# Performance work log

Measured on AMD Instinct MI355X. Metric: run time of the kernel, lower is better.

Reference implementation:

```python
import jax, jax.numpy as jnp
import numpy as np

S_DIM = 8      # state_dim
O_DIM = 4      # obs_dim
HID = (S_DIM * S_DIM + O_DIM * O_DIM) * 10   # 800
BATCH = 128
SEQ = 32
NS = 16        # num_samples
P_DROP = 0.2
DROP_KEY = jax.random.key(42)

def f_dyn(x):
    # synthetic nonlinear dynamics (stand-in for system_model.f, vmapped over batch)
    return 0.9 * x + 0.1 * jnp.sin(x)

def h_obs(x):
    # synthetic nonlinear observation (stand-in for system_model.h)
    return jnp.tanh(x[..., :O_DIM])

def l2_normalize(x, eps=1e-12):
    # matches torch F.normalize(p=2, dim=1): x / max(||x||, eps)
    n = jnp.linalg.norm(x, axis=-1, keepdims=True)
    return x / jnp.maximum(n, eps)

def setup_inputs() -> dict:
    key = jax.random.key(0)
    ks = jax.random.split(key, 8)
    g = 0.02
    return {
        "y_seq": jax.random.normal(ks[0], (BATCH, SEQ, O_DIM), dtype=jnp.float32),
        "W1": jax.random.normal(ks[1], (HID, S_DIM + O_DIM), dtype=jnp.float32) * g,
        "b1": jnp.zeros((HID,), jnp.float32),
        "W_ih": jax.random.normal(ks[2], (3 * HID, HID), dtype=jnp.float32) * g,
        "W_hh": jax.random.normal(ks[3], (3 * HID, HID), dtype=jnp.float32) * g,
        "b_ih": jnp.zeros((3 * HID,), jnp.float32),
        "b_hh": jnp.zeros((3 * HID,), jnp.float32),
        "W_out": jax.random.normal(ks[4], (S_DIM * O_DIM, HID), dtype=jnp.float32) * g,
        "b_out": jnp.zeros((S_DIM * O_DIM,), jnp.float32),
        "num_samples": NS,
    }

def _forward(y_seq, W1, b1, W_ih, W_hh, b_ih, b_hh, W_out, b_out, num_samples):
    B = y_seq.shape[0]
    keep = 1.0 - P_DROP

    def gru_cell(x, h):
        # torch nn.GRU single-step math; x,h: [..., HID]
        gi = x @ W_ih.T + b_ih
        gh = h @ W_hh.T + b_hh
        gi_r, gi_z, gi_n = jnp.split(gi, 3, axis=-1)
        gh_r, gh_z, gh_n = jnp.split(gh, 3, axis=-1)
        r = jax.nn.sigmoid(gi_r + gh_r)
        z = jax.nn.sigmoid(gi_z + gh_z)
        n = jnp.tanh(gi_n + r * gh_n)
        return (1.0 - z) * n + z * h

    def step(carry, inp):
        x_prev, dx_prev, h_ens = carry            # [B,S], [B,S], [NS,B,HID]
        y_t, t = inp
        x_pred = f_dyn(x_prev)                    # [B,S] (same for every sample j)
        y_hat = h_obs(x_pred)                     # [B,O]
        innov = y_t - y_hat                       # [B,O]
        nn_in = jnp.concatenate([l2_normalize(dx_prev), l2_normalize(innov)], axis=-1)
        a = jax.nn.relu(nn_in @ W1.T + b1)        # [B,HID]
        k1, k2 = jax.random.split(jax.random.fold_in(DROP_KEY, t))
        m1 = jax.random.bernoulli(k1, keep, (num_samples, B, HID)).astype(a.dtype)
        a_ens = a[None] * m1 / keep               # MC-dropout per ensemble member
        h_new = gru_cell(a_ens, h_ens)            # [NS,B,HID] (vectorized over samples)
        K_vec = h_new @ W_out.T + b_out           # [NS,B,S*O]
        m2 = jax.random.bernoulli(k2, keep, K_vec.shape).astype(a.dtype)
        K = (K_vec * m2 / keep).reshape(num_samples, B, S_DIM, O_DIM)
        ens = x_pred[None] + jnp.einsum('jbso,bo->jbs', K, innov)  # [NS,B,S]
        x_filt = ens.mean(axis=0)                 # [B,S]
        diff = ens - x_filt[None]                 # [NS,B,S]
        P_filt = jnp.einsum('jbs,jbt->bst', diff, diff) / num_samples
        dx = x_filt - x_pred                      # delta_x_prev = x_filt - f(x_prev)
        return (x_filt, dx, h_new), (x_filt, P_filt)

    x0 = jnp.zeros((B, S_DIM), y_seq.dtype)
    dx0 = jnp.zeros((B, S_DIM), y_seq.dtype)
    h0 = jnp.zeros((num_samples, B, HID), y_seq.dtype)
    ts = jnp.arange(y_seq.shape[1])
    _, (xs, Ps) = jax.lax.scan(step, (x0, dx0, h0), (jnp.swapaxes(y_seq, 0, 1), ts))
    # xs: [T,B,S] -> [B,T,S]; Ps: [T,B,S,S] -> [B,T,S,S]
    return jnp.swapaxes(xs, 0, 1), jnp.swapaxes(Ps, 0, 1)

def reference(y_seq, W1, b1, W_ih, W_hh, b_ih, b_hh, W_out, b_out, num_samples):
    return _forward(y_seq, W1, b1, W_ih, W_hh, b_ih, b_hh, W_out, b_out, num_samples)
```

## Files before the change

kernel.cpp:

```cpp
#include <hip/hip_runtime.h>
#include <stdint.h>

#define NSAMP 16
#define BATCH 128
#define SEQLEN 32
#define SDIM 8
#define ODIM 4
#define HID 800
#define MROWS (NSAMP * BATCH)
#define KEEPP 0.8f

#define WPK_NBLK 77824
#define WPK_G 12928
#define WPK_C 808
#define GRU_LDS_BYTES 155648

typedef __attribute__((ext_vector_type(8))) short short8v;
typedef __attribute__((ext_vector_type(4))) float float4v;

__host__ __device__ __forceinline__ void tf2x32(uint32_t k0, uint32_t k1,
                                                uint32_t x0, uint32_t x1,
                                                uint32_t& o0, uint32_t& o1) {
  uint32_t ks2 = k0 ^ k1 ^ 0x1BD11BDAu;
  x0 += k0; x1 += k1;
#define TFR(r) { x0 += x1; x1 = (x1 << (r)) | (x1 >> (32 - (r))); x1 ^= x0; }
  TFR(13) TFR(15) TFR(26) TFR(6)
  x0 += k1; x1 += ks2 + 1u;
  TFR(17) TFR(29) TFR(16) TFR(24)
  x0 += ks2; x1 += k0 + 2u;
  TFR(13) TFR(15) TFR(26) TFR(6)
  x0 += k0; x1 += k1 + 3u;
  TFR(17) TFR(29) TFR(16) TFR(24)
  x0 += k1; x1 += ks2 + 4u;
  TFR(13) TFR(15) TFR(26) TFR(6)
  x0 += ks2; x1 += k0 + 5u;
#undef TFR
  o0 = x0; o1 = x1;
}

__device__ __forceinline__ float bits_to_unit(uint32_t bits) {
  return __uint_as_float((bits >> 9) | 0x3F800000u) - 1.0f;
}

__device__ __forceinline__ float tf_uniform_part(uint32_t k0, uint32_t k1, uint32_t idx) {
  uint32_t b1, b2;
  tf2x32(k0, k1, 0u, idx, b1, b2);
  return bits_to_unit(b1 ^ b2);
}

__device__ __forceinline__ ushort f2bf(float f) {
  uint32_t u = __float_as_uint(f);
  uint32_t r = (u + 0x7FFFu + ((u >> 16) & 1u)) >> 16;
  return (ushort)r;
}

__device__ __forceinline__ float bf2f(ushort u) {
  return __uint_as_float((uint32_t)u << 16);
}

__global__ void pack_w_kernel(const float* __restrict__ W_ih, const float* __restrict__ W_hh,
                              ushort* __restrict__ Wpk) {
  const int blk = blockIdx.x;
  const int nblk = blk / 6, g = blk % 6;
  const float* W = (g < 3) ? W_ih : W_hh;
  const int grow = (g % 3) * HID;
  ushort* dst = Wpk + (size_t)nblk * WPK_NBLK + (size_t)g * WPK_G;
  for (int idx = threadIdx.x; idx < 16 * WPK_C; idx += 256) {
    int c = idx / WPK_C, k = idx - c * WPK_C;
    float v = (k < HID) ? W[(size_t)(grow + nblk * 16 + c) * HID + k] : 0.0f;
    dst[c * WPK_C + k] = f2bf(v);
  }
}

__global__ void transpose_wout_kernel(const float* __restrict__ W_out, float* __restrict__ WoutT) {
  int i = blockIdx.x * 256 + threadIdx.x;
  if (i < 32 * HID) {
    int o = i / HID, k = i - o * HID;
    WoutT[k * 32 + o] = W_out[i];
  }
}

__global__ void a_ens_kernel(const float* __restrict__ a, ushort* __restrict__ aeb,
                             uint32_t k0, uint32_t k1) {
  int base = (blockIdx.x * blockDim.x + threadIdx.x) * 4;
  if (base >= MROWS * HID) return;
  int row = base / HID;
  int b = row % BATCH;
  int col = base - row * HID;
  float4 av = *reinterpret_cast<const float4*>(a + b * HID + col);
  ushort4 ov;
#pragma unroll
  for (int q = 0; q < 4; ++q) {
    float u = tf_uniform_part(k0, k1, (uint32_t)(base + q));
    float f = (&av.x)[q] * ((u < KEEPP) ? 1.25f : 0.0f);
    (&ov.x)[q] = f2bf(f);
  }
  *reinterpret_cast<ushort4*>(aeb + base) = ov;
}

__global__ __launch_bounds__(512, 2) void gru_mfma_kernel(
    const ushort* __restrict__ aeb, const ushort* __restrict__ hb,
    const ushort* __restrict__ Wpk,
    const float* __restrict__ h_old,
    const float* __restrict__ b_ih, const float* __restrict__ b_hh,
    float* __restrict__ h_new, ushort* __restrict__ h_new_b) {
  extern __shared__ __align__(16) char lds[];

  const int tid = threadIdx.x;
  const int w = tid >> 6;
  const int lane = tid & 63;
  const int l15 = lane & 15;
  const int kg = lane >> 4;

  const int bid = blockIdx.x;
  const int nhalf = bid >> 3;
  const int r3 = bid & 7;
  const int mblk = r3 >> 1;
  const int nblk = nhalf * 2 + (r3 & 1);
  const int m0 = mblk * 512;
  const int n0 = nblk * 16;

  {
    const ushort* wsrc = Wpk + (size_t)nblk * WPK_NBLK + (size_t)lane * 8;
    for (int s = w * 19; s < w * 19 + 19; ++s) {
      __builtin_amdgcn_global_load_lds(
          (const __attribute__((address_space(1))) void*)(wsrc + (size_t)s * 512),
          (__attribute__((address_space(3))) void*)(lds + s * 1024), 16, 0, 0);
    }
  }

  float4v acc[6][4];
#pragma unroll
  for (int g = 0; g < 6; ++g)
#pragma unroll
    for (int mf = 0; mf < 4; ++mf)
      acc[g][mf] = (float4v)(0.0f);

  const ushort* ap[2][4];
#pragma unroll
  for (int mf = 0; mf < 4; ++mf) {
    const int row = m0 + w * 64 + mf * 16 + l15;
    ap[0][mf] = aeb + (size_t)row * HID + kg * 8;
    ap[1][mf] = hb + (size_t)row * HID + kg * 8;
  }
  short8v ar0[2][4], ar1[2][4];

#define LOADA(SET) do {                                                          \
    _Pragma("unroll")                                                            \
    for (int s2 = 0; s2 < 2; ++s2)                                               \
      _Pragma("unroll")                                                          \
      for (int mf = 0; mf < 4; ++mf) {                                           \
        SET[s2][mf] = *reinterpret_cast<const short8v*>(ap[s2][mf]);             \
        ap[s2][mf] += 32;                                                        \
      }                                                                          \
  } while (0)

#define COMP(T, SET) do {                                                        \
    short8v bfr[6];                                                              \
    _Pragma("unroll")                                                            \
    for (int g = 0; g < 6; ++g)                                                  \
      bfr[g] = *reinterpret_cast<const short8v*>(                                \
          lds + g * 25856 + l15 * 1616 + (T) * 64 + kg * 16);                    \
    __builtin_amdgcn_s_setprio(1);                                               \
    _Pragma("unroll")                                                            \
    for (int g = 0; g < 6; ++g) {                                                \
      const int src = (g < 3) ? 0 : 1;                                           \
      _Pragma("unroll")                                                          \
      for (int mf = 0; mf < 4; ++mf)                                             \
        acc[g][mf] = __builtin_amdgcn_mfma_f32_16x16x32_bf16(                    \
            SET[src][mf], bfr[g], acc[g][mf], 0, 0, 0);                          \
    }                                                                            \
    __builtin_amdgcn_s_setprio(0);                                               \
  } while (0)

  LOADA(ar0);
  asm volatile("s_waitcnt vmcnt(0)" ::: "memory");
  __syncthreads();

#pragma unroll 1
  for (int t = 0; t < 24; t += 2) {
    LOADA(ar1);
    COMP(t, ar0);
    LOADA(ar0);
    COMP(t + 1, ar1);
  }
  COMP(24, ar0);

  const int rowq = (lane >> 4) * 4;
  const int col = n0 + l15;
  const float bir = b_ih[col], biz = b_ih[col + HID], bin = b_ih[col + 2 * HID];
  const float bhr = b_hh[col], bhz = b_hh[col + HID], bhn = b_hh[col + 2 * HID];
#pragma unroll
  for (int mf = 0; mf < 4; ++mf) {
#pragma unroll
    for (int reg = 0; reg < 4; ++reg) {
      const int m = m0 + w * 64 + mf * 16 + rowq + reg;
      float gir = acc[0][mf][reg] + bir;
      float giz = acc[1][mf][reg] + biz;
      float gin = acc[2][mf][reg] + bin;
      float ghr = acc[3][mf][reg] + bhr;
      float ghz = acc[4][mf][reg] + bhz;
      float ghn = acc[5][mf][reg] + bhn;
      float r = 1.0f / (1.0f + expf(-(gir + ghr)));
      float z = 1.0f / (1.0f + expf(-(giz + ghz)));
      float nval = tanhf(gin + r * ghn);
      float hv = h_old[(size_t)m * HID + col];
      float res = (1.0f - z) * nval + z * hv;
      h_new[(size_t)m * HID + col] = res;
      h_new_b[(size_t)m * HID + col] = f2bf(res);
    }
  }
#undef LOADA
#undef COMP
}

__global__ void kvec_ens_kernel(const ushort* __restrict__ hnb,
                                const float* __restrict__ WoutT,
                                const float* __restrict__ b_out,
                                const float* __restrict__ x_pred,
                                const float* __restrict__ innov,
                                float* __restrict__ ens,
                                uint32_t k0, uint32_t k1) {
  const int jb = blockIdx.x;
  const int b = jb & (BATCH - 1);
  const int tid = threadIdx.x;
  const int o = tid & 31;
  const int kk = tid >> 5;

  const ushort* hrow = hnb + (size_t)jb * HID + kk * 100;
  const float* wc = WoutT + kk * 100 * 32 + o;
  float partial = 0.0f;
  for (int k = 0; k < 100; ++k)
    partial = fmaf(bf2f(hrow[k]), wc[k * 32], partial);

  __shared__ float red[8][32];
  __shared__ float Kv[32];
  red[kk][o] = partial;
  __syncthreads();
  if (tid < 32) {
    float s = 0.0f;
#pragma unroll
    for (int q = 0; q < 8; ++q) s += red[q][tid];
    s += b_out[tid];
    float u = tf_uniform_part(k0, k1, (uint32_t)(jb * 32 + tid));
    Kv[tid] = (u < KEEPP) ? s * 1.25f : 0.0f;
  }
  __syncthreads();
  if (tid < SDIM) {
    float s = x_pred[b * SDIM + tid];
#pragma unroll
    for (int oo = 0; oo < ODIM; ++oo)
      s = fmaf(Kv[tid * ODIM + oo], innov[b * ODIM + oo], s);
    ens[jb * SDIM + tid] = s;
  }
}

__global__ void reduce_prep_kernel(const float* __restrict__ ens,
                                   float* __restrict__ x_pred,
                                   float* __restrict__ innov,
                                   const float* __restrict__ y_seq,
                                   const float* __restrict__ W1,
                                   const float* __restrict__ b1,
                                   float* __restrict__ a,
                                   float* __restrict__ out_xs, float* __restrict__ out_Ps,
                                   int t) {
  const int b = blockIdx.x;
  const int tid = threadIdx.x;
  __shared__ float e[NSAMP][SDIM];
  __shared__ float xf[SDIM];
  __shared__ float dxs[SDIM];
  __shared__ float xpn[SDIM];
  __shared__ float inv[ODIM];
  __shared__ float nin[SDIM + ODIM];

  if (t >= 0) {
    if (tid < NSAMP * SDIM) {
      int j = tid >> 3, s = tid & 7;
      e[j][s] = ens[(j * BATCH + b) * SDIM + s];
    }
    __syncthreads();
    if (tid < SDIM) {
      float s = 0.0f;
#pragma unroll
      for (int j = 0; j < NSAMP; ++j) s += e[j][tid];
      s *= (1.0f / NSAMP);
      xf[tid] = s;
      out_xs[(b * SEQLEN + t) * SDIM + tid] = s;
      dxs[tid] = s - x_pred[b * SDIM + tid];
    }
    __syncthreads();
    if (tid < SDIM * SDIM) {
      int s = tid >> 3, u = tid & 7;
      float accv = 0.0f;
#pragma unroll
      for (int j = 0; j < NSAMP; ++j)
        accv += (e[j][s] - xf[s]) * (e[j][u] - xf[u]);
      out_Ps[((b * SEQLEN + t) * SDIM + s) * SDIM + u] = accv * (1.0f / NSAMP);
    }
  } else {
    if (tid < SDIM) { xf[tid] = 0.0f; dxs[tid] = 0.0f; }
  }
  if (t == SEQLEN - 1) return;
  __syncthreads();
  if (tid < SDIM) {
    float x = xf[tid];
    float xp = 0.9f * x + 0.1f * sinf(x);
    xpn[tid] = xp;
    x_pred[b * SDIM + tid] = xp;
  }
  __syncthreads();
  if (tid < ODIM) {
    float yh = tanhf(xpn[tid]);
    float iv = y_seq[(b * SEQLEN + (t + 1)) * ODIM + tid] - yh;
    inv[tid] = iv;
    innov[b * ODIM + tid] = iv;
  }
  __syncthreads();
  if (tid == 0) {
    float nd = 0.0f;
    for (int s = 0; s < SDIM; ++s) nd += dxs[s] * dxs[s];
    nd = fmaxf(sqrtf(nd), 1e-12f);
    for (int s = 0; s < SDIM; ++s) nin[s] = dxs[s] / nd;
    float ni = 0.0f;
    for (int o2 = 0; o2 < ODIM; ++o2) ni += inv[o2] * inv[o2];
    ni = fmaxf(sqrtf(ni), 1e-12f);
    for (int o2 = 0; o2 < ODIM; ++o2) nin[SDIM + o2] = inv[o2] / ni;
  }
  __syncthreads();
  for (int i = tid; i < HID; i += blockDim.x) {
    float s = b1[i];
#pragma unroll
    for (int c = 0; c < 12; ++c) s = fmaf(nin[c], W1[i * 12 + c], s);
    a[b * HID + i] = fmaxf(s, 0.0f);
  }
}

extern "C" void kernel_launch(void* const* d_in, const int* in_sizes, int n_in,
                              void* d_out, int out_size, void* d_ws, size_t ws_size,
                              hipStream_t stream) {
  (void)in_sizes; (void)n_in; (void)out_size; (void)ws_size;
  const float* y_seq = (const float*)d_in[0];
  const float* W1 = (const float*)d_in[1];
  const float* b1 = (const float*)d_in[2];
  const float* W_ih = (const float*)d_in[3];
  const float* W_hh = (const float*)d_in[4];
  const float* b_ih = (const float*)d_in[5];
  const float* b_hh = (const float*)d_in[6];
  const float* W_out = (const float*)d_in[7];
  const float* b_out = (const float*)d_in[8];

  char* ws = (char*)d_ws;
  size_t off = 0;
  float* h_a = (float*)(ws + off);    off += (size_t)MROWS * HID * 4;
  float* h_b = (float*)(ws + off);    off += (size_t)MROWS * HID * 4;
  ushort* hb_a = (ushort*)(ws + off); off += (size_t)MROWS * HID * 2;
  ushort* hb_b = (ushort*)(ws + off); off += (size_t)MROWS * HID * 2;
  ushort* aeb = (ushort*)(ws + off);  off += (size_t)MROWS * HID * 2;
  ushort* Wpk = (ushort*)(ws + off);  off += (size_t)50 * WPK_NBLK * 2;
  float* a_buf = (float*)(ws + off);  off += (size_t)BATCH * HID * 4;
  float* WoutT = (float*)(ws + off);  off += (size_t)HID * 32 * 4;
  float* x_pred = (float*)(ws + off); off += (size_t)BATCH * SDIM * 4;
  float* innov = (float*)(ws + off);  off += (size_t)BATCH * ODIM * 4;
  float* ens = (float*)(ws + off);    off += (size_t)NSAMP * BATCH * SDIM * 4;

  float* out_xs = (float*)d_out;
  float* out_Ps = out_xs + (size_t)BATCH * SEQLEN * SDIM;

  (void)hipFuncSetAttribute(reinterpret_cast<const void*>(&gru_mfma_kernel),
                            hipFuncAttributeMaxDynamicSharedMemorySize, GRU_LDS_BYTES);

  hipMemsetAsync(h_a, 0, (size_t)MROWS * HID * 4, stream);
  hipMemsetAsync(hb_a, 0, (size_t)MROWS * HID * 2, stream);
  pack_w_kernel<<<300, 256, 0, stream>>>(W_ih, W_hh, Wpk);
  transpose_wout_kernel<<<100, 256, 0, stream>>>(W_out, WoutT);
  reduce_prep_kernel<<<BATCH, 256, 0, stream>>>(ens, x_pred, innov, y_seq, W1, b1,
                                                a_buf, out_xs, out_Ps, -1);

  float* hc = h_a;  float* hn = h_b;
  ushort* hcb = hb_a; ushort* hnb = hb_b;
  for (int t = 0; t < SEQLEN; ++t) {
    uint32_t kt0, kt1, k1a, k1b, k2a, k2b;
    tf2x32(0u, 42u, 0u, (uint32_t)t, kt0, kt1);
    tf2x32(kt0, kt1, 0u, 0u, k1a, k1b);
    tf2x32(kt0, kt1, 0u, 1u, k2a, k2b);

    a_ens_kernel<<<1600, 256, 0, stream>>>(a_buf, aeb, k1a, k1b);
    gru_mfma_kernel<<<200, 512, GRU_LDS_BYTES, stream>>>(aeb, hcb, Wpk, hc,
                                                         b_ih, b_hh, hn, hnb);
    kvec_ens_kernel<<<MROWS, 256, 0, stream>>>(hnb, WoutT, b_out, x_pred, innov, ens, k2a, k2b);
    reduce_prep_kernel<<<BATCH, 256, 0, stream>>>(ens, x_pred, innov, y_seq, W1, b1,
                                                  a_buf, out_xs, out_Ps, t);
    float* tmp = hc; hc = hn; hn = tmp;
    ushort* tmpb = hcb; hcb = hnb; hnb = tmpb;
  }
}
```

Baseline: 2.043 ms.

## Store GRU A-operands in MFMA fragment order and deepen load pipeline

```diff
diff --git a/kernel.cpp b/kernel.cpp
--- a/kernel.cpp
+++ b/kernel.cpp
@@ -54,10 +54,6 @@
   return (ushort)r;
 }
 
-__device__ __forceinline__ float bf2f(ushort u) {
-  return __uint_as_float((uint32_t)u << 16);
-}
-
 __global__ void pack_w_kernel(const float* __restrict__ W_ih, const float* __restrict__ W_hh,
                               ushort* __restrict__ Wpk) {
   const int blk = blockIdx.x;
@@ -80,30 +76,39 @@
   }
 }
 
-__global__ void a_ens_kernel(const float* __restrict__ a, ushort* __restrict__ aeb,
+__global__ void a_ens_kernel(const float* __restrict__ a_buf, ushort* __restrict__ AF,
                              uint32_t k0, uint32_t k1) {
-  int base = (blockIdx.x * blockDim.x + threadIdx.x) * 4;
-  if (base >= MROWS * HID) return;
-  int row = base / HID;
-  int b = row % BATCH;
-  int col = base - row * HID;
-  float4 av = *reinterpret_cast<const float4*>(a + b * HID + col);
-  ushort4 ov;
+  const int gw = blockIdx.x * 4 + (threadIdx.x >> 6);
+  const int lane = threadIdx.x & 63;
+  const int mt = gw / 25, kt = gw - mt * 25;
+  const int row = mt * 16 + (lane & 15);
+  const int b = row & (BATCH - 1);
+  const int k = kt * 32 + (lane >> 4) * 8;
+  const float* src = a_buf + (size_t)b * HID + k;
+  float4 v0 = *reinterpret_cast<const float4*>(src);
+  float4 v1 = *reinterpret_cast<const float4*>(src + 4);
+  const uint32_t base = (uint32_t)(row * HID + k);
+  ushort o[8];
 #pragma unroll
   for (int q = 0; q < 4; ++q) {
-    float u = tf_uniform_part(k0, k1, (uint32_t)(base + q));
-    float f = (&av.x)[q] * ((u < KEEPP) ? 1.25f : 0.0f);
-    (&ov.x)[q] = f2bf(f);
-  }
-  *reinterpret_cast<ushort4*>(aeb + base) = ov;
+    float u = tf_uniform_part(k0, k1, base + q);
+    o[q] = f2bf((&v0.x)[q] * ((u < KEEPP) ? 1.25f : 0.0f));
+  }
+#pragma unroll
+  for (int q = 0; q < 4; ++q) {
+    float u = tf_uniform_part(k0, k1, base + 4 + q);
+    o[4 + q] = f2bf((&v1.x)[q] * ((u < KEEPP) ? 1.25f : 0.0f));
+  }
+  *reinterpret_cast<short8v*>(AF + ((size_t)gw * 64 + lane) * 8) =
+      *reinterpret_cast<const short8v*>(o);
 }
 
 __global__ __launch_bounds__(512, 2) void gru_mfma_kernel(
-    const ushort* __restrict__ aeb, const ushort* __restrict__ hb,
+    const ushort* __restrict__ AF, const ushort* __restrict__ HF,
     const ushort* __restrict__ Wpk,
     const float* __restrict__ h_old,
     const float* __restrict__ b_ih, const float* __restrict__ b_hh,
-    float* __restrict__ h_new, ushort* __restrict__ h_new_b) {
+    float* __restrict__ h_new, ushort* __restrict__ hf_out) {
   extern __shared__ __align__(16) char lds[];
 
   const int tid = threadIdx.x;
@@ -119,6 +124,7 @@
   const int nblk = nhalf * 2 + (r3 & 1);
   const int m0 = mblk * 512;
   const int n0 = nblk * 16;
+  const int mtb = mblk * 32;
 
   {
     const ushort* wsrc = Wpk + (size_t)nblk * WPK_NBLK + (size_t)lane * 8;
@@ -139,19 +145,19 @@
   const ushort* ap[2][4];
 #pragma unroll
   for (int mf = 0; mf < 4; ++mf) {
-    const int row = m0 + w * 64 + mf * 16 + l15;
-    ap[0][mf] = aeb + (size_t)row * HID + kg * 8;
-    ap[1][mf] = hb + (size_t)row * HID + kg * 8;
-  }
-  short8v ar0[2][4], ar1[2][4];
+    const size_t mt = (size_t)(mtb + w * 4 + mf);
+    ap[0][mf] = AF + mt * 12800 + (size_t)lane * 8;
+    ap[1][mf] = HF + mt * 12800 + (size_t)lane * 8;
+  }
+  short8v s0[2][4], s1[2][4], s2[2][4];
 
 #define LOADA(SET) do {                                                          \
     _Pragma("unroll")                                                            \
-    for (int s2 = 0; s2 < 2; ++s2)                                               \
+    for (int sx = 0; sx < 2; ++sx)                                               \
       _Pragma("unroll")                                                          \
       for (int mf = 0; mf < 4; ++mf) {                                           \
-        SET[s2][mf] = *reinterpret_cast<const short8v*>(ap[s2][mf]);             \
-        ap[s2][mf] += 32;                                                        \
+        SET[sx][mf] = *reinterpret_cast<const short8v*>(ap[sx][mf]);             \
+        ap[sx][mf] += 512;                                                       \
       }                                                                          \
   } while (0)
 
@@ -173,25 +179,44 @@
     __builtin_amdgcn_s_setprio(0);                                               \
   } while (0)
 
-  LOADA(ar0);
+  LOADA(s0);
+  LOADA(s1);
+  asm volatile("s_waitcnt vmcnt(16)" ::: "memory");
+  __syncthreads();
+
+#pragma unroll 1
+  for (int t = 0; t < 21; t += 3) {
+    LOADA(s2);
+    asm volatile("s_waitcnt vmcnt(16)" ::: "memory");
+    COMP(t, s0);
+    LOADA(s0);
+    asm volatile("s_waitcnt vmcnt(16)" ::: "memory");
+    COMP(t + 1, s1);
+    LOADA(s1);
+    asm volatile("s_waitcnt vmcnt(16)" ::: "memory");
+    COMP(t + 2, s2);
+  }
+  LOADA(s2);
+  asm volatile("s_waitcnt vmcnt(16)" ::: "memory");
+  COMP(21, s0);
+  LOADA(s0);
+  asm volatile("s_waitcnt vmcnt(16)" ::: "memory");
+  COMP(22, s1);
+  asm volatile("s_waitcnt vmcnt(8)" ::: "memory");
+  COMP(23, s2);
   asm volatile("s_waitcnt vmcnt(0)" ::: "memory");
-  __syncthreads();
-
-#pragma unroll 1
-  for (int t = 0; t < 24; t += 2) {
-    LOADA(ar1);
-    COMP(t, ar0);
-    LOADA(ar0);
-    COMP(t + 1, ar1);
-  }
-  COMP(24, ar0);
+  COMP(24, s0);
 
   const int rowq = (lane >> 4) * 4;
   const int col = n0 + l15;
   const float bir = b_ih[col], biz = b_ih[col + HID], bin = b_ih[col + 2 * HID];
   const float bhr = b_hh[col], bhz = b_hh[col + HID], bhn = b_hh[col + 2 * HID];
+  const int khalf = (l15 >> 3) & 1;
+  const int kq = l15 & 7;
 #pragma unroll
   for (int mf = 0; mf < 4; ++mf) {
+    const size_t mt = (size_t)(mtb + w * 4 + mf);
+    ushort* hfw = hf_out + mt * 12800 + (size_t)nblk * 256 + khalf * 128 + kq;
 #pragma unroll
     for (int reg = 0; reg < 4; ++reg) {
       const int m = m0 + w * 64 + mf * 16 + rowq + reg;
@@ -207,14 +232,14 @@
       float hv = h_old[(size_t)m * HID + col];
       float res = (1.0f - z) * nval + z * hv;
       h_new[(size_t)m * HID + col] = res;
-      h_new_b[(size_t)m * HID + col] = f2bf(res);
+      hfw[(rowq + reg) * 8] = f2bf(res);
     }
   }
 #undef LOADA
 #undef COMP
 }
 
-__global__ void kvec_ens_kernel(const ushort* __restrict__ hnb,
+__global__ void kvec_ens_kernel(const float* __restrict__ h_new,
                                 const float* __restrict__ WoutT,
                                 const float* __restrict__ b_out,
                                 const float* __restrict__ x_pred,
@@ -227,11 +252,10 @@
   const int o = tid & 31;
   const int kk = tid >> 5;
 
-  const ushort* hrow = hnb + (size_t)jb * HID + kk * 100;
-  const float* wc = WoutT + kk * 100 * 32 + o;
+  const float* hrow = h_new + (size_t)jb * HID;
   float partial = 0.0f;
-  for (int k = 0; k < 100; ++k)
-    partial = fmaf(bf2f(hrow[k]), wc[k * 32], partial);
+  for (int k = kk * 100; k < kk * 100 + 100; ++k)
+    partial = fmaf(hrow[k], WoutT[k * 32 + o], partial);
 
   __shared__ float red[8][32];
   __shared__ float Kv[32];
@@ -353,9 +377,9 @@
   size_t off = 0;
   float* h_a = (float*)(ws + off);    off += (size_t)MROWS * HID * 4;
   float* h_b = (float*)(ws + off);    off += (size_t)MROWS * HID * 4;
-  ushort* hb_a = (ushort*)(ws + off); off += (size_t)MROWS * HID * 2;
-  ushort* hb_b = (ushort*)(ws + off); off += (size_t)MROWS * HID * 2;
-  ushort* aeb = (ushort*)(ws + off);  off += (size_t)MROWS * HID * 2;
+  ushort* hf_a = (ushort*)(ws + off); off += (size_t)MROWS * HID * 2;
+  ushort* hf_b = (ushort*)(ws + off); off += (size_t)MROWS * HID * 2;
+  ushort* AF = (ushort*)(ws + off);   off += (size_t)MROWS * HID * 2;
   ushort* Wpk = (ushort*)(ws + off);  off += (size_t)50 * WPK_NBLK * 2;
   float* a_buf = (float*)(ws + off);  off += (size_t)BATCH * HID * 4;
   float* WoutT = (float*)(ws + off);  off += (size_t)HID * 32 * 4;
@@ -370,27 +394,27 @@
                             hipFuncAttributeMaxDynamicSharedMemorySize, GRU_LDS_BYTES);
 
   hipMemsetAsync(h_a, 0, (size_t)MROWS * HID * 4, stream);
-  hipMemsetAsync(hb_a, 0, (size_t)MROWS * HID * 2, stream);
+  hipMemsetAsync(hf_a, 0, (size_t)MROWS * HID * 2, stream);
   pack_w_kernel<<<300, 256, 0, stream>>>(W_ih, W_hh, Wpk);
   transpose_wout_kernel<<<100, 256, 0, stream>>>(W_out, WoutT);
   reduce_prep_kernel<<<BATCH, 256, 0, stream>>>(ens, x_pred, innov, y_seq, W1, b1,
                                                 a_buf, out_xs, out_Ps, -1);
 
   float* hc = h_a;  float* hn = h_b;
-  ushort* hcb = hb_a; ushort* hnb = hb_b;
+  ushort* hfc = hf_a; ushort* hfn = hf_b;
   for (int t = 0; t < SEQLEN; ++t) {
     uint32_t kt0, kt1, k1a, k1b, k2a, k2b;
     tf2x32(0u, 42u, 0u, (uint32_t)t, kt0, kt1);
     tf2x32(kt0, kt1, 0u, 0u, k1a, k1b);
     tf2x32(kt0, kt1, 0u, 1u, k2a, k2b);
 
-    a_ens_kernel<<<1600, 256, 0, stream>>>(a_buf, aeb, k1a, k1b);
-    gru_mfma_kernel<<<200, 512, GRU_LDS_BYTES, stream>>>(aeb, hcb, Wpk, hc,
-                                                         b_ih, b_hh, hn, hnb);
-    kvec_ens_kernel<<<MROWS, 256, 0, stream>>>(hnb, WoutT, b_out, x_pred, innov, ens, k2a, k2b);
+    a_ens_kernel<<<800, 256, 0, stream>>>(a_buf, AF, k1a, k1b);
+    gru_mfma_kernel<<<200, 512, GRU_LDS_BYTES, stream>>>(AF, hfc, Wpk, hc,
+                                                         b_ih, b_hh, hn, hfn);
+    kvec_ens_kernel<<<MROWS, 256, 0, stream>>>(hn, WoutT, b_out, x_pred, innov, ens, k2a, k2b);
     reduce_prep_kernel<<<BATCH, 256, 0, stream>>>(ens, x_pred, innov, y_seq, W1, b1,
                                                   a_buf, out_xs, out_Ps, t);
     float* tmp = hc; hc = hn; hn = tmp;
-    ushort* tmpb = hcb; hcb = hnb; hnb = tmpb;
-  }
-}
+    ushort* tmpf = hfc; hfc = hfn; hfn = tmpf;
+  }
+}
```

Measured after the change: 1.735 ms. 15.1% less time.
